# Kernel optimization log

Measured on AMD Instinct MI355X. Metric: run time of the kernel, lower is better.

Reference implementation:

```python
import jax, jax.numpy as jnp
import numpy as np

N = 50000
E_RAND = 800000
F_IN = 128
H = 4          # num_heads
D_HID = 32     # hidden per-head dim
D_OUT = 32     # output per-head dim
NEG_SLOPE_ATTN = 0.2   # DGL GATConv attention leaky_relu
NEG_SLOPE_ACT = 0.01   # F.leaky_relu default activation


def setup_inputs() -> dict:
    key = jax.random.key(0)
    ks = jax.random.split(key, 12)
    x = jax.random.normal(ks[0], (N, F_IN), dtype=jnp.float32)
    src_r = jax.random.randint(ks[1], (E_RAND,), 0, N, dtype=jnp.int32)
    dst_r = jax.random.randint(ks[2], (E_RAND,), 0, N, dtype=jnp.int32)
    loop = jnp.arange(N, dtype=jnp.int32)
    src = jnp.concatenate([src_r, loop])  # add_self_loop
    dst = jnp.concatenate([dst_r, loop])
    sc1 = 1.0 / np.sqrt(F_IN)
    sc2 = 1.0 / np.sqrt(H * D_HID)
    W1 = jax.random.normal(ks[3], (F_IN, H * D_HID), dtype=jnp.float32) * sc1
    al1 = jax.random.normal(ks[4], (H, D_HID), dtype=jnp.float32) * sc1
    ar1 = jax.random.normal(ks[5], (H, D_HID), dtype=jnp.float32) * sc1
    b1 = jnp.zeros((H * D_HID,), dtype=jnp.float32)
    W2 = jax.random.normal(ks[6], (H * D_HID, H * D_OUT), dtype=jnp.float32) * sc2
    al2 = jax.random.normal(ks[7], (H, D_OUT), dtype=jnp.float32) * sc2
    ar2 = jax.random.normal(ks[8], (H, D_OUT), dtype=jnp.float32) * sc2
    b2 = jnp.zeros((H * D_OUT,), dtype=jnp.float32)
    return {"x": x, "src": src, "dst": dst,
            "W1": W1, "al1": al1, "ar1": ar1, "b1": b1,
            "W2": W2, "al2": al2, "ar2": ar2, "b2": b2}


def gat_conv(x, src, dst, W, al, ar, b, act_slope):
    n = x.shape[0]
    h, d = al.shape
    feat = (x @ W).reshape(n, h, d)                 # [N,H,D]
    el = jnp.einsum('nhd,hd->nh', feat, al)         # [N,H]
    er = jnp.einsum('nhd,hd->nh', feat, ar)
    # edge attention score on edge u->v: leaky_relu(el[u] + er[v])
    e = jax.nn.leaky_relu(el[src] + er[dst], NEG_SLOPE_ATTN)  # [E,H]
    # edge softmax over incoming edges of each dst node (self-loops guarantee >=1 edge)
    m = jax.ops.segment_max(e, dst, num_segments=n)           # [N,H]
    ex = jnp.exp(e - m[dst])
    s = jax.ops.segment_sum(ex, dst, num_segments=n)
    a = ex / s[dst]                                           # [E,H]
    # attention-weighted scatter-sum of source features
    out = jax.ops.segment_sum(a[:, :, None] * feat[src], dst, num_segments=n)  # [N,H,D]
    out = out + b.reshape(h, d)
    if act_slope is not None:
        out = jax.nn.leaky_relu(out, act_slope)
    return out.reshape(n, h * d)                    # flatten(1)


def reference(x, src, dst, W1, al1, ar1, b1, W2, al2, ar2, b2):
    h = gat_conv(x, src, dst, W1, al1, ar1, b1, NEG_SLOPE_ACT)
    out = gat_conv(h, src, dst, W2, al2, ar2, b2, None)  # last layer: no activation
    return out
```

## Files before the change

### kernel.cpp

```cpp
#include <hip/hip_runtime.h>
#include <hip/hip_bf16.h>
#include <hip/hip_fp16.h>

#define HEADS 4
#define DHEAD 32
#define FDIM 128
#define BCAP 64
#define RPB 64
#define XPAD (FDIM/4 + 1)

typedef float nfloat4 __attribute__((ext_vector_type(4)));

__device__ __forceinline__ void gemm_body(
    const float* __restrict__ X, const float* __restrict__ W,
    const float* __restrict__ al, const float* __restrict__ ar,
    __half* __restrict__ feat, float* __restrict__ el, float* __restrict__ er,
    int n, float* Xs) {
    int r0 = blockIdx.x * RPB;
    int rowsLeft = n - r0; if (rowsLeft > RPB) rowsLeft = RPB;
    {
        nfloat4* xsw = (nfloat4*)Xs;
        const nfloat4* Xg = (const nfloat4*)(X + (size_t)r0 * FDIM);
        for (int i = threadIdx.x; i < RPB * (FDIM / 4); i += 256) {
            int row = i >> 5, c4 = i & 31;
            int sr = row < rowsLeft ? row : 0;
            xsw[row * XPAD + c4] =
                __builtin_nontemporal_load(&Xg[(size_t)sr * (FDIM / 4) + c4]);
        }
    }
    __syncthreads();

    int head = __builtin_amdgcn_readfirstlane(threadIdx.x >> 6);
    int lane = threadIdx.x & 63;
    int row = r0 + lane;
    bool valid = row < n;

    const float4* xs4 = (const float4*)Xs + (size_t)lane * XPAD;
    const float* wb = W + head * DHEAD;

    float acc[32];
#pragma unroll
    for (int j = 0; j < 32; j++) acc[j] = 0.f;

#pragma unroll 4
    for (int k4 = 0; k4 < FDIM / 4; k4++) {
        float4 a = xs4[k4];
#pragma unroll
        for (int kk = 0; kk < 4; kk++) {
            const float4* wr = (const float4*)(wb + (size_t)(k4 * 4 + kk) * FDIM);
            float s = (&a.x)[kk];
#pragma unroll
            for (int j4 = 0; j4 < 8; j4++) {
                float4 wv = wr[j4];
                acc[j4 * 4 + 0] += s * wv.x;
                acc[j4 * 4 + 1] += s * wv.y;
                acc[j4 * 4 + 2] += s * wv.z;
                acc[j4 * 4 + 3] += s * wv.w;
            }
        }
    }

    float elv = 0.f, erv = 0.f;
#pragma unroll
    for (int j = 0; j < 32; j++) {
        elv += acc[j] * al[head * DHEAD + j];
        erv += acc[j] * ar[head * DHEAD + j];
    }
    if (valid) {
        el[(size_t)row * HEADS + head] = elv;
        er[(size_t)row * HEADS + head] = erv;
    }

    if (valid) {
        union { __half2 h2[16]; uint4 u4[4]; } pk;
#pragma unroll
        for (int m = 0; m < 16; m++)
            pk.h2[m] = __floats2half2_rn(acc[2 * m], acc[2 * m + 1]);
        uint4* dstp = (uint4*)(feat + (size_t)row * FDIM + head * DHEAD);
#pragma unroll
        for (int t = 0; t < 4; t++) dstp[t] = pk.u4[t];
    }
}

__global__ __launch_bounds__(256) void k_gemm_l1(
    const float* __restrict__ X, const float* __restrict__ W,
    const float* __restrict__ al, const float* __restrict__ ar,
    __half* __restrict__ feat, float* __restrict__ el, float* __restrict__ er, int n,
    const int* __restrict__ esrc, const int* __restrict__ edst,
    int* __restrict__ deg, ushort* __restrict__ bucket, int E) {
    __shared__ float Xs[RPB * 4 * XPAD];

    {
        int nb = gridDim.x;
        int echunk = (E + nb - 1) / nb;
        int e0 = blockIdx.x * echunk;
        int e1 = e0 + echunk; if (e1 > E) e1 = E;
        for (int base = e0 + threadIdx.x; base < e1; base += 256 * 8) {
            int d[8], s[8], p[8];
#pragma unroll
            for (int j = 0; j < 8; j++) {
                int idx = base + j * 256;
                if (idx < e1) {
                    d[j] = __builtin_nontemporal_load(&edst[idx]);
                    s[j] = __builtin_nontemporal_load(&esrc[idx]);
                } else d[j] = -1;
            }
#pragma unroll
            for (int j = 0; j < 8; j++)
                if (d[j] >= 0) p[j] = atomicAdd(&deg[d[j]], 1);
#pragma unroll
            for (int j = 0; j < 8; j++)
                if (d[j] >= 0 && p[j] < BCAP)
                    bucket[((size_t)d[j] << 6) + p[j]] = (ushort)s[j];
        }
    }

    gemm_body(X, W, al, ar, feat, el, er, n, Xs);
}

__global__ __launch_bounds__(256) void k_gemm_l2(
    const float* __restrict__ X, const float* __restrict__ W,
    const float* __restrict__ al, const float* __restrict__ ar,
    __half* __restrict__ feat, float* __restrict__ el, float* __restrict__ er, int n) {
    __shared__ float Xs[RPB * 4 * XPAD];
    gemm_body(X, W, al, ar, feat, el, er, n, Xs);
}

__device__ __forceinline__ void agg_body(
    const ushort* __restrict__ bucket, const int* __restrict__ deg,
    const __half2* __restrict__ feat2h, const float* __restrict__ el,
    const float* __restrict__ er, const float* __restrict__ b,
    float* __restrict__ out, int n, int apply_act) {
    int wave = threadIdx.x >> 6;
    int node = blockIdx.x * 4 + wave;
    if (node >= n) return;
    node = __builtin_amdgcn_readfirstlane(node);
    int lane = threadIdx.x & 63;
    int h = lane >> 4;

    float ern = er[(size_t)node * HEADS + h];
    int cnt = __builtin_amdgcn_readfirstlane(deg[node]);
    const ushort* bkt = bucket + ((size_t)node << 6);

    float ax = 0.f, ay = 0.f, sw = 0.f;
    int i = 0;

    for (; i + 8 <= cnt; i += 8) {
        int s[8];
#pragma unroll
        for (int j = 0; j < 8; j++) s[j] = (int)bkt[i + j];
        float e[8];
#pragma unroll
        for (int j = 0; j < 8; j++) e[j] = el[(size_t)s[j] * HEADS + h];
        __half2 f[8];
#pragma unroll
        for (int j = 0; j < 8; j++) f[j] = feat2h[(size_t)s[j] * 64 + lane];
#pragma unroll
        for (int j = 0; j < 8; j++) {
            float ev = e[j] + ern;
            ev = ev > 0.f ? ev : 0.2f * ev;
            float w = __expf(ev);
            float2 fv = __half22float2(f[j]);
            sw += w; ax += w * fv.x; ay += w * fv.y;
        }
    }
    for (; i + 2 <= cnt; i += 2) {
        int s0 = (int)bkt[i], s1 = (int)bkt[i + 1];
        float e0 = el[(size_t)s0 * HEADS + h];
        float e1 = el[(size_t)s1 * HEADS + h];
        __half2 f0 = feat2h[(size_t)s0 * 64 + lane];
        __half2 f1 = feat2h[(size_t)s1 * 64 + lane];
        e0 += ern; e0 = e0 > 0.f ? e0 : 0.2f * e0;
        e1 += ern; e1 = e1 > 0.f ? e1 : 0.2f * e1;
        float w0 = __expf(e0), w1 = __expf(e1);
        float2 fv0 = __half22float2(f0), fv1 = __half22float2(f1);
        sw += w0 + w1;
        ax += w0 * fv0.x + w1 * fv1.x;
        ay += w0 * fv0.y + w1 * fv1.y;
    }
    if (i < cnt) {
        int s0 = (int)bkt[i];
        float e0 = el[(size_t)s0 * HEADS + h] + ern;
        e0 = e0 > 0.f ? e0 : 0.2f * e0;
        float w0 = __expf(e0);
        float2 fv0 = __half22float2(feat2h[(size_t)s0 * 64 + lane]);
        sw += w0; ax += w0 * fv0.x; ay += w0 * fv0.y;
    }

    float inv = 1.0f / sw;
    float2 bv = ((const float2*)b)[lane];
    float ox = ax * inv + bv.x;
    float oy = ay * inv + bv.y;
    if (apply_act) {
        ox = ox > 0.f ? ox : 0.01f * ox;
        oy = oy > 0.f ? oy : 0.01f * oy;
    }
    float2 o; o.x = ox; o.y = oy;
    ((float2*)out)[(size_t)node * 64 + lane] = o;
}

__global__ __launch_bounds__(256) void k_agg_l1(
    const ushort* __restrict__ bucket, const int* __restrict__ deg,
    const __half2* __restrict__ feat2h, const float* __restrict__ el,
    const float* __restrict__ er, const float* __restrict__ b,
    float* __restrict__ out, int n) {
    agg_body(bucket, deg, feat2h, el, er, b, out, n, 1);
}

__global__ __launch_bounds__(256) void k_agg_l2(
    const ushort* __restrict__ bucket, const int* __restrict__ deg,
    const __half2* __restrict__ feat2h, const float* __restrict__ el,
    const float* __restrict__ er, const float* __restrict__ b,
    float* __restrict__ out, int n) {
    agg_body(bucket, deg, feat2h, el, er, b, out, n, 0);
}


extern "C" void kernel_launch(void* const* d_in, const int* in_sizes, int n_in,
                              void* d_out, int out_size, void* d_ws, size_t ws_size,
                              hipStream_t stream) {
    const float* x   = (const float*)d_in[0];
    const int*   src = (const int*)d_in[1];
    const int*   dst = (const int*)d_in[2];
    const float* W1  = (const float*)d_in[3];
    const float* al1 = (const float*)d_in[4];
    const float* ar1 = (const float*)d_in[5];
    const float* b1  = (const float*)d_in[6];
    const float* W2  = (const float*)d_in[7];
    const float* al2 = (const float*)d_in[8];
    const float* ar2 = (const float*)d_in[9];
    const float* b2  = (const float*)d_in[10];
    int N = in_sizes[0] / FDIM;
    int E = in_sizes[1];
    float* out = (float*)d_out;

    __half* featA  = (__half*)d_ws;
    float*  elb    = (float*)(featA + (size_t)N * FDIM);
    float*  erb    = elb + (size_t)N * HEADS;
    int*    deg    = (int*)(erb + (size_t)N * HEADS);
    ushort* bucket = (ushort*)(deg + N);
    float*  hbuf   = out;

    int gblocks = (N + RPB - 1) / RPB;

    (void)hipMemsetAsync(deg, 0, (size_t)N * sizeof(int), stream);

    k_gemm_l1<<<gblocks, 256, 0, stream>>>(x, W1, al1, ar1, featA, elb, erb, N,
                                           src, dst, deg, bucket, E);
    k_agg_l1<<<(N + 3) / 4, 256, 0, stream>>>(bucket, deg, (const __half2*)featA,
                                              elb, erb, b1, hbuf, N);

    k_gemm_l2<<<gblocks, 256, 0, stream>>>(hbuf, W2, al2, ar2, featA, elb, erb, N);
    k_agg_l2<<<(N + 3) / 4, 256, 0, stream>>>(bucket, deg, (const __half2*)featA,
                                              elb, erb, b2, out, N);
}
```

Measured before the change: 275.4 us.

## Store features head-major and aggregate one head per block with padded degree counters

Features and attention logits are stored head-major ([H][N][D]) instead of node-major. The aggregation grid is remapped so each block handles a single head across interleaved node ranges, with each wave splitting a node's edges by parity across its two 32-lane halves and combining them with a cross-lane shuffle. Degree counters are padded to one per 64-byte stride to reduce atomic contention and false sharing. The head-major layout is meant to keep each head's gathered working set smaller and more cache-resident, but each gather now reads only 64 bytes, half the lanes idle on the store, and the degree memset grows sixteenfold.

```diff
diff --git a/kernel.cpp b/kernel.cpp
--- a/kernel.cpp
+++ b/kernel.cpp
@@ -8,13 +8,14 @@
 #define BCAP 64
 #define RPB 64
 #define XPAD (FDIM/4 + 1)
+#define DEGPAD 16
 
 typedef float nfloat4 __attribute__((ext_vector_type(4)));
 
 __device__ __forceinline__ void gemm_body(
     const float* __restrict__ X, const float* __restrict__ W,
     const float* __restrict__ al, const float* __restrict__ ar,
-    __half* __restrict__ feat, float* __restrict__ el, float* __restrict__ er,
+    __half* __restrict__ feat, float* __restrict__ el2, float* __restrict__ er2,
     int n, float* Xs) {
     int r0 = blockIdx.x * RPB;
     int rowsLeft = n - r0; if (rowsLeft > RPB) rowsLeft = RPB;
@@ -67,8 +68,8 @@
         erv += acc[j] * ar[head * DHEAD + j];
     }
     if (valid) {
-        el[(size_t)row * HEADS + head] = elv;
-        er[(size_t)row * HEADS + head] = erv;
+        el2[(size_t)head * n + row] = elv;
+        er2[(size_t)head * n + row] = erv;
     }
 
     if (valid) {
@@ -76,7 +77,7 @@
 #pragma unroll
         for (int m = 0; m < 16; m++)
             pk.h2[m] = __floats2half2_rn(acc[2 * m], acc[2 * m + 1]);
-        uint4* dstp = (uint4*)(feat + (size_t)row * FDIM + head * DHEAD);
+        uint4* dstp = (uint4*)(feat + ((size_t)head * n + row) * DHEAD);
 #pragma unroll
         for (int t = 0; t < 4; t++) dstp[t] = pk.u4[t];
     }
@@ -85,9 +86,9 @@
 __global__ __launch_bounds__(256) void k_gemm_l1(
     const float* __restrict__ X, const float* __restrict__ W,
     const float* __restrict__ al, const float* __restrict__ ar,
-    __half* __restrict__ feat, float* __restrict__ el, float* __restrict__ er, int n,
+    __half* __restrict__ feat, float* __restrict__ el2, float* __restrict__ er2, int n,
     const int* __restrict__ esrc, const int* __restrict__ edst,
-    int* __restrict__ deg, ushort* __restrict__ bucket, int E) {
+    int* __restrict__ degp, ushort* __restrict__ bucket, int E) {
     __shared__ float Xs[RPB * 4 * XPAD];
 
     {
@@ -107,7 +108,7 @@
             }
 #pragma unroll
             for (int j = 0; j < 8; j++)
-                if (d[j] >= 0) p[j] = atomicAdd(&deg[d[j]], 1);
+                if (d[j] >= 0) p[j] = atomicAdd(&degp[(size_t)d[j] * DEGPAD], 1);
 #pragma unroll
             for (int j = 0; j < 8; j++)
                 if (d[j] >= 0 && p[j] < BCAP)
@@ -115,104 +116,91 @@
         }
     }
 
-    gemm_body(X, W, al, ar, feat, el, er, n, Xs);
+    gemm_body(X, W, al, ar, feat, el2, er2, n, Xs);
 }
 
 __global__ __launch_bounds__(256) void k_gemm_l2(
     const float* __restrict__ X, const float* __restrict__ W,
     const float* __restrict__ al, const float* __restrict__ ar,
-    __half* __restrict__ feat, float* __restrict__ el, float* __restrict__ er, int n) {
+    __half* __restrict__ feat, float* __restrict__ el2, float* __restrict__ er2, int n) {
     __shared__ float Xs[RPB * 4 * XPAD];
-    gemm_body(X, W, al, ar, feat, el, er, n, Xs);
+    gemm_body(X, W, al, ar, feat, el2, er2, n, Xs);
 }
 
 __device__ __forceinline__ void agg_body(
-    const ushort* __restrict__ bucket, const int* __restrict__ deg,
-    const __half2* __restrict__ feat2h, const float* __restrict__ el,
-    const float* __restrict__ er, const float* __restrict__ b,
+    const ushort* __restrict__ bucket, const int* __restrict__ degp,
+    const __half* __restrict__ feat, const float* __restrict__ el2,
+    const float* __restrict__ er2, const float* __restrict__ b,
     float* __restrict__ out, int n, int apply_act) {
+    int nb4 = (n + 3) >> 2;
+    int per_sub = (nb4 + 1) >> 1;
+    int slot = blockIdx.x & 7;
+    int h = slot >> 1, sub = slot & 1;
+    int j = blockIdx.x >> 3;
+    int nodeblock = sub * per_sub + j;
     int wave = threadIdx.x >> 6;
-    int node = blockIdx.x * 4 + wave;
-    if (node >= n) return;
+    int node = nodeblock * 4 + wave;
+    if (nodeblock >= nb4 || node >= n) return;
     node = __builtin_amdgcn_readfirstlane(node);
     int lane = threadIdx.x & 63;
-    int h = lane >> 4;
-
-    float ern = er[(size_t)node * HEADS + h];
-    int cnt = __builtin_amdgcn_readfirstlane(deg[node]);
+    int f = lane & 31;
+    int parity = lane >> 5;
+
+    size_t hN = (size_t)h * n;
+    float ern = er2[hN + node];
+    int cnt = __builtin_amdgcn_readfirstlane(degp[(size_t)node * DEGPAD]);
     const ushort* bkt = bucket + ((size_t)node << 6);
-
-    float ax = 0.f, ay = 0.f, sw = 0.f;
-    int i = 0;
-
-    for (; i + 8 <= cnt; i += 8) {
-        int s[8];
-#pragma unroll
-        for (int j = 0; j < 8; j++) s[j] = (int)bkt[i + j];
-        float e[8];
-#pragma unroll
-        for (int j = 0; j < 8; j++) e[j] = el[(size_t)s[j] * HEADS + h];
-        __half2 f[8];
-#pragma unroll
-        for (int j = 0; j < 8; j++) f[j] = feat2h[(size_t)s[j] * 64 + lane];
-#pragma unroll
-        for (int j = 0; j < 8; j++) {
-            float ev = e[j] + ern;
-            ev = ev > 0.f ? ev : 0.2f * ev;
-            float w = __expf(ev);
-            float2 fv = __half22float2(f[j]);
-            sw += w; ax += w * fv.x; ay += w * fv.y;
-        }
-    }
-    for (; i + 2 <= cnt; i += 2) {
-        int s0 = (int)bkt[i], s1 = (int)bkt[i + 1];
-        float e0 = el[(size_t)s0 * HEADS + h];
-        float e1 = el[(size_t)s1 * HEADS + h];
-        __half2 f0 = feat2h[(size_t)s0 * 64 + lane];
-        __half2 f1 = feat2h[(size_t)s1 * 64 + lane];
-        e0 += ern; e0 = e0 > 0.f ? e0 : 0.2f * e0;
-        e1 += ern; e1 = e1 > 0.f ? e1 : 0.2f * e1;
-        float w0 = __expf(e0), w1 = __expf(e1);
-        float2 fv0 = __half22float2(f0), fv1 = __half22float2(f1);
-        sw += w0 + w1;
-        ax += w0 * fv0.x + w1 * fv1.x;
-        ay += w0 * fv0.y + w1 * fv1.y;
-    }
-    if (i < cnt) {
-        int s0 = (int)bkt[i];
-        float e0 = el[(size_t)s0 * HEADS + h] + ern;
-        e0 = e0 > 0.f ? e0 : 0.2f * e0;
-        float w0 = __expf(e0);
-        float2 fv0 = __half22float2(feat2h[(size_t)s0 * 64 + lane]);
-        sw += w0; ax += w0 * fv0.x; ay += w0 * fv0.y;
-    }
-
-    float inv = 1.0f / sw;
-    float2 bv = ((const float2*)b)[lane];
-    float ox = ax * inv + bv.x;
-    float oy = ay * inv + bv.y;
-    if (apply_act) {
-        ox = ox > 0.f ? ox : 0.01f * ox;
-        oy = oy > 0.f ? oy : 0.01f * oy;
-    }
-    float2 o; o.x = ox; o.y = oy;
-    ((float2*)out)[(size_t)node * 64 + lane] = o;
+    const float* elh = el2 + hN;
+    const __half* fh = feat + hN * DHEAD;
+
+    float ax = 0.f, sw = 0.f;
+    int kmax = (cnt + 1) >> 1;
+    for (int k = 0; k < kmax; k += 4) {
+        int s[4]; bool vld[4];
+#pragma unroll
+        for (int u = 0; u < 4; u++) {
+            int e = 2 * (k + u) + parity;
+            vld[u] = e < cnt;
+            s[u] = vld[u] ? (int)bkt[e] : 0;
+        }
+        float ev[4];
+#pragma unroll
+        for (int u = 0; u < 4; u++) ev[u] = elh[s[u]];
+        __half fv[4];
+#pragma unroll
+        for (int u = 0; u < 4; u++) fv[u] = fh[(size_t)s[u] * DHEAD + f];
+#pragma unroll
+        for (int u = 0; u < 4; u++) {
+            float t = ev[u] + ern;
+            t = t > 0.f ? t : 0.2f * t;
+            float w = vld[u] ? __expf(t) : 0.f;
+            sw += w;
+            ax += w * __half2float(fv[u]);
+        }
+    }
+    sw += __shfl_xor(sw, 32, 64);
+    ax += __shfl_xor(ax, 32, 64);
+
+    float o = ax / sw + b[h * DHEAD + f];
+    if (apply_act) o = o > 0.f ? o : 0.01f * o;
+    if (parity == 0)
+        out[(size_t)node * FDIM + h * DHEAD + f] = o;
 }
 
 __global__ __launch_bounds__(256) void k_agg_l1(
-    const ushort* __restrict__ bucket, const int* __restrict__ deg,
-    const __half2* __restrict__ feat2h, const float* __restrict__ el,
-    const float* __restrict__ er, const float* __restrict__ b,
+    const ushort* __restrict__ bucket, const int* __restrict__ degp,
+    const __half* __restrict__ feat, const float* __restrict__ el2,
+    const float* __restrict__ er2, const float* __restrict__ b,
     float* __restrict__ out, int n) {
-    agg_body(bucket, deg, feat2h, el, er, b, out, n, 1);
+    agg_body(bucket, degp, feat, el2, er2, b, out, n, 1);
 }
 
 __global__ __launch_bounds__(256) void k_agg_l2(
-    const ushort* __restrict__ bucket, const int* __restrict__ deg,
-    const __half2* __restrict__ feat2h, const float* __restrict__ el,
-    const float* __restrict__ er, const float* __restrict__ b,
+    const ushort* __restrict__ bucket, const int* __restrict__ degp,
+    const __half* __restrict__ feat, const float* __restrict__ el2,
+    const float* __restrict__ er2, const float* __restrict__ b,
     float* __restrict__ out, int n) {
-    agg_body(bucket, deg, feat2h, el, er, b, out, n, 0);
+    agg_body(bucket, degp, feat, el2, er2, b, out, n, 0);
 }
 
 
@@ -235,22 +223,23 @@
     float* out = (float*)d_out;
 
     __half* featA  = (__half*)d_ws;
-    float*  elb    = (float*)(featA + (size_t)N * FDIM);
-    float*  erb    = elb + (size_t)N * HEADS;
-    int*    deg    = (int*)(erb + (size_t)N * HEADS);
-    ushort* bucket = (ushort*)(deg + N);
+    float*  el2b   = (float*)(featA + (size_t)N * FDIM);
+    float*  er2b   = el2b + (size_t)HEADS * N;
+    int*    degp   = (int*)(er2b + (size_t)HEADS * N);
+    ushort* bucket = (ushort*)(degp + (size_t)N * DEGPAD);
     float*  hbuf   = out;
 
     int gblocks = (N + RPB - 1) / RPB;
-
-    (void)hipMemsetAsync(deg, 0, (size_t)N * sizeof(int), stream);
-
-    k_gemm_l1<<<gblocks, 256, 0, stream>>>(x, W1, al1, ar1, featA, elb, erb, N,
-                                           src, dst, deg, bucket, E);
-    k_agg_l1<<<(N + 3) / 4, 256, 0, stream>>>(bucket, deg, (const __half2*)featA,
-                                              elb, erb, b1, hbuf, N);
-
-    k_gemm_l2<<<gblocks, 256, 0, stream>>>(hbuf, W2, al2, ar2, featA, elb, erb, N);
-    k_agg_l2<<<(N + 3) / 4, 256, 0, stream>>>(bucket, deg, (const __half2*)featA,
-                                              elb, erb, b2, out, N);
-}
+    int nb4 = (N + 3) / 4;
+    int per_sub = (nb4 + 1) / 2;
+    int agrid = 8 * per_sub;
+
+    (void)hipMemsetAsync(degp, 0, (size_t)N * DEGPAD * sizeof(int), stream);
+
+    k_gemm_l1<<<gblocks, 256, 0, stream>>>(x, W1, al1, ar1, featA, el2b, er2b, N,
+                                           src, dst, degp, bucket, E);
+    k_agg_l1<<<agrid, 256, 0, stream>>>(bucket, degp, featA, el2b, er2b, b1, hbuf, N);
+
+    k_gemm_l2<<<gblocks, 256, 0, stream>>>(hbuf, W2, al2, ar2, featA, el2b, er2b, N);
+    k_agg_l2<<<agrid, 256, 0, stream>>>(bucket, degp, featA, el2b, er2b, b2, out, N);
+}
```

Result: slower. 433.1 us (+57.3%).

## Pad degree counters and precompute per-edge attention weights in LDS

Applied to the files above, without the earlier changes.

Degree counters are spread to one per 64-byte stride to cut atomic contention on shared cache lines, at the cost of a larger memset and workspace. The aggregation kernel first computes all edge softmax weights for a node in parallel across lanes (each lane handles bucket slots for one head) and stores them in shared memory. The main loop then reads packed pairs of source indices as 32-bit words and pulls the weights from LDS, so the serial per-edge exp and el gather disappear. It also clamps the count to the bucket capacity and reads out-of-range bucket slots with index clamping, which adds wasted loads for low-degree nodes.

```diff
diff --git a/kernel.cpp b/kernel.cpp
--- a/kernel.cpp
+++ b/kernel.cpp
@@ -8,6 +8,8 @@
 #define BCAP 64
 #define RPB 64
 #define XPAD (FDIM/4 + 1)
+#define DEGPAD 16
+#define WSTRIDE 68
 
 typedef float nfloat4 __attribute__((ext_vector_type(4)));
 
@@ -87,7 +89,7 @@
     const float* __restrict__ al, const float* __restrict__ ar,
     __half* __restrict__ feat, float* __restrict__ el, float* __restrict__ er, int n,
     const int* __restrict__ esrc, const int* __restrict__ edst,
-    int* __restrict__ deg, ushort* __restrict__ bucket, int E) {
+    int* __restrict__ degp, ushort* __restrict__ bucket, int E) {
     __shared__ float Xs[RPB * 4 * XPAD];
 
     {
@@ -107,7 +109,7 @@
             }
 #pragma unroll
             for (int j = 0; j < 8; j++)
-                if (d[j] >= 0) p[j] = atomicAdd(&deg[d[j]], 1);
+                if (d[j] >= 0) p[j] = atomicAdd(&degp[(size_t)d[j] * DEGPAD], 1);
 #pragma unroll
             for (int j = 0; j < 8; j++)
                 if (d[j] >= 0 && p[j] < BCAP)
@@ -127,64 +129,74 @@
 }
 
 __device__ __forceinline__ void agg_body(
-    const ushort* __restrict__ bucket, const int* __restrict__ deg,
+    const ushort* __restrict__ bucket, const int* __restrict__ degp,
     const __half2* __restrict__ feat2h, const float* __restrict__ el,
     const float* __restrict__ er, const float* __restrict__ b,
     float* __restrict__ out, int n, int apply_act) {
+    __shared__ float ws_all[4][HEADS * WSTRIDE];
     int wave = threadIdx.x >> 6;
     int node = blockIdx.x * 4 + wave;
     if (node >= n) return;
     node = __builtin_amdgcn_readfirstlane(node);
     int lane = threadIdx.x & 63;
+    float* ws = ws_all[wave];
+
+    int cnt = __builtin_amdgcn_readfirstlane(degp[(size_t)node * DEGPAD]);
+    if (cnt > BCAP) cnt = BCAP;
+    const ushort* bkt = bucket + ((size_t)node << 6);
+
+    {
+        int ph = lane >> 4;
+        int sl = lane & 15;
+        float ern = er[(size_t)node * HEADS + ph];
+        int slot[4]; float ev[4];
+#pragma unroll
+        for (int bb = 0; bb < 4; bb++) {
+            slot[bb] = bb * 16 + sl;
+            int s = (int)bkt[slot[bb]];
+            if (s >= n) s = 0;
+            ev[bb] = el[(size_t)s * HEADS + ph];
+        }
+#pragma unroll
+        for (int bb = 0; bb < 4; bb++) {
+            float t = ev[bb] + ern;
+            t = t > 0.f ? t : 0.2f * t;
+            float w = (slot[bb] < cnt) ? __expf(t) : 0.f;
+            ws[ph * WSTRIDE + slot[bb]] = w;
+        }
+    }
+    asm volatile("s_waitcnt lgkmcnt(0)" ::: "memory");
+
     int h = lane >> 4;
-
-    float ern = er[(size_t)node * HEADS + h];
-    int cnt = __builtin_amdgcn_readfirstlane(deg[node]);
-    const ushort* bkt = bucket + ((size_t)node << 6);
-
+    const float2* wsh2 = (const float2*)(ws + h * WSTRIDE);
+    const uint* bp32 = (const uint*)bkt;
     float ax = 0.f, ay = 0.f, sw = 0.f;
-    int i = 0;
-
-    for (; i + 8 <= cnt; i += 8) {
-        int s[8];
-#pragma unroll
-        for (int j = 0; j < 8; j++) s[j] = (int)bkt[i + j];
-        float e[8];
-#pragma unroll
-        for (int j = 0; j < 8; j++) e[j] = el[(size_t)s[j] * HEADS + h];
-        __half2 f[8];
-#pragma unroll
-        for (int j = 0; j < 8; j++) f[j] = feat2h[(size_t)s[j] * 64 + lane];
-#pragma unroll
-        for (int j = 0; j < 8; j++) {
-            float ev = e[j] + ern;
-            ev = ev > 0.f ? ev : 0.2f * ev;
-            float w = __expf(ev);
-            float2 fv = __half22float2(f[j]);
-            sw += w; ax += w * fv.x; ay += w * fv.y;
-        }
-    }
-    for (; i + 2 <= cnt; i += 2) {
-        int s0 = (int)bkt[i], s1 = (int)bkt[i + 1];
-        float e0 = el[(size_t)s0 * HEADS + h];
-        float e1 = el[(size_t)s1 * HEADS + h];
-        __half2 f0 = feat2h[(size_t)s0 * 64 + lane];
-        __half2 f1 = feat2h[(size_t)s1 * 64 + lane];
-        e0 += ern; e0 = e0 > 0.f ? e0 : 0.2f * e0;
-        e1 += ern; e1 = e1 > 0.f ? e1 : 0.2f * e1;
-        float w0 = __expf(e0), w1 = __expf(e1);
-        float2 fv0 = __half22float2(f0), fv1 = __half22float2(f1);
-        sw += w0 + w1;
-        ax += w0 * fv0.x + w1 * fv1.x;
-        ay += w0 * fv0.y + w1 * fv1.y;
-    }
-    if (i < cnt) {
-        int s0 = (int)bkt[i];
-        float e0 = el[(size_t)s0 * HEADS + h] + ern;
-        e0 = e0 > 0.f ? e0 : 0.2f * e0;
-        float w0 = __expf(e0);
-        float2 fv0 = __half22float2(feat2h[(size_t)s0 * 64 + lane]);
-        sw += w0; ax += w0 * fv0.x; ay += w0 * fv0.y;
+    int pairs = (cnt + 1) >> 1;
+    for (int k0 = 0; k0 < pairs; k0 += 4) {
+        uint pk[4];
+#pragma unroll
+        for (int u = 0; u < 4; u++) {
+            int kk = k0 + u;
+            pk[u] = __builtin_amdgcn_readfirstlane(kk < pairs ? bp32[kk] : 0u);
+        }
+        __half2 f[8]; float2 w2[4];
+#pragma unroll
+        for (int u = 0; u < 4; u++) {
+            int s0 = (int)(pk[u] & 0xffffu), s1 = (int)(pk[u] >> 16);
+            if (s0 >= n) s0 = 0;
+            if (s1 >= n) s1 = 0;
+            f[2 * u]     = feat2h[(size_t)s0 * 64 + lane];
+            f[2 * u + 1] = feat2h[(size_t)s1 * 64 + lane];
+            w2[u] = wsh2[k0 + u];
+        }
+#pragma unroll
+        for (int u = 0; u < 4; u++) {
+            float2 f0 = __half22float2(f[2 * u]);
+            float2 f1 = __half22float2(f[2 * u + 1]);
+            sw += w2[u].x + w2[u].y;
+            ax += w2[u].x * f0.x + w2[u].y * f1.x;
+            ay += w2[u].x * f0.y + w2[u].y * f1.y;
+        }
     }
 
     float inv = 1.0f / sw;
@@ -200,19 +212,19 @@
 }
 
 __global__ __launch_bounds__(256) void k_agg_l1(
-    const ushort* __restrict__ bucket, const int* __restrict__ deg,
+    const ushort* __restrict__ bucket, const int* __restrict__ degp,
     const __half2* __restrict__ feat2h, const float* __restrict__ el,
     const float* __restrict__ er, const float* __restrict__ b,
     float* __restrict__ out, int n) {
-    agg_body(bucket, deg, feat2h, el, er, b, out, n, 1);
+    agg_body(bucket, degp, feat2h, el, er, b, out, n, 1);
 }
 
 __global__ __launch_bounds__(256) void k_agg_l2(
-    const ushort* __restrict__ bucket, const int* __restrict__ deg,
+    const ushort* __restrict__ bucket, const int* __restrict__ degp,
     const __half2* __restrict__ feat2h, const float* __restrict__ el,
     const float* __restrict__ er, const float* __restrict__ b,
     float* __restrict__ out, int n) {
-    agg_body(bucket, deg, feat2h, el, er, b, out, n, 0);
+    agg_body(bucket, degp, feat2h, el, er, b, out, n, 0);
 }
 
 
@@ -237,20 +249,21 @@
     __half* featA  = (__half*)d_ws;
     float*  elb    = (float*)(featA + (size_t)N * FDIM);
     float*  erb    = elb + (size_t)N * HEADS;
-    int*    deg    = (int*)(erb + (size_t)N * HEADS);
-    ushort* bucket = (ushort*)(deg + N);
+    int*    degp   = (int*)(erb + (size_t)N * HEADS);
+    ushort* bucket = (ushort*)(degp + (size_t)N * DEGPAD);
     float*  hbuf   = out;
 
     int gblocks = (N + RPB - 1) / RPB;
-
-    (void)hipMemsetAsync(deg, 0, (size_t)N * sizeof(int), stream);
+    int ablocks = (N + 3) / 4;
+
+    (void)hipMemsetAsync(degp, 0, (size_t)N * DEGPAD * sizeof(int), stream);
 
     k_gemm_l1<<<gblocks, 256, 0, stream>>>(x, W1, al1, ar1, featA, elb, erb, N,
-                                           src, dst, deg, bucket, E);
-    k_agg_l1<<<(N + 3) / 4, 256, 0, stream>>>(bucket, deg, (const __half2*)featA,
-                                              elb, erb, b1, hbuf, N);
+                                           src, dst, degp, bucket, E);
+    k_agg_l1<<<ablocks, 256, 0, stream>>>(bucket, degp, (const __half2*)featA,
+                                          elb, erb, b1, hbuf, N);
 
     k_gemm_l2<<<gblocks, 256, 0, stream>>>(hbuf, W2, al2, ar2, featA, elb, erb, N);
-    k_agg_l2<<<(N + 3) / 4, 256, 0, stream>>>(bucket, deg, (const __half2*)featA,
-                                              elb, erb, b2, out, N);
-}
+    k_agg_l2<<<ablocks, 256, 0, stream>>>(bucket, degp, (const __half2*)featA,
+                                          elb, erb, b2, out, N);
+}
```

Result: no change. 274.5 us (-0.3%).
